# Performance work log

Measured on AMD Instinct MI355X. Metric: run time of the kernel, lower is better.

## Reference

```python
import jax, jax.numpy as jnp
import numpy as np

TOPK = 5
POWER = 1.01


def setup_inputs() -> dict:
    key = jax.random.key(0)
    k1, k2 = jax.random.split(key)
    B, C = 16384, 8192
    inp = jax.random.normal(k1, (B, C), dtype=jnp.float32)
    target = jax.random.randint(k2, (B,), 0, C, dtype=jnp.int64 if jax.config.jax_enable_x64 else jnp.int32)
    return {"input": inp, "target": target}


def reference(input, target):
    B = input.shape[0]
    rows = jnp.arange(B)
    # log(softmax(x)) == log_softmax(x)
    log_prob = jax.nn.log_softmax(input, axis=-1)  # [B, C]
    # top-k selection over classes
    topk_vals, topk_idx = jax.lax.top_k(input, TOPK)  # [B, K]
    # custom power-based softmax on the top-k subset
    exp_in = jnp.power(jnp.asarray(POWER, input.dtype), topk_vals)  # [B, K]
    log_prob_topk = jnp.log(exp_in / jnp.sum(exp_in, axis=-1, keepdims=True))
    # scatter the top-k log-probs back into a copy of log_prob
    log_prob_copy = log_prob.at[rows[:, None], topk_idx].set(log_prob_topk)
    # gather-based cross-entropy terms
    loss1 = jnp.mean(-log_prob[rows, target])
    loss2 = jnp.mean(-log_prob_copy[rows, target])
    return loss1 + loss2
```

## Files before the change

kernel.cpp:

```cpp
#include <hip/hip_runtime.h>

#define BLOCK 256
#define NCHUNK 8
#define NC 8192

__device__ __forceinline__ float fexp2(float x) { return __builtin_amdgcn_exp2f(x); }
__device__ __forceinline__ float flog2(float x) { return __builtin_amdgcn_logf(x); }

__device__ __forceinline__ void cas(float& hi, float& lo) {
    float h = fmaxf(hi, lo), l = fminf(hi, lo);
    hi = h; lo = l;
}

__device__ __forceinline__ void sort5(float& a0, float& a1, float& a2, float& a3, float& a4) {
    cas(a0, a1); cas(a3, a4); cas(a2, a4); cas(a2, a3); cas(a1, a4);
    cas(a0, a3); cas(a0, a2); cas(a1, a3); cas(a1, a2);
}

__device__ __forceinline__ void merge55(float& a0, float& a1, float& a2, float& a3, float& a4,
                                        float b0, float b1, float b2, float b3, float b4) {
    float L0 = fmaxf(a0, b4);
    float L1 = fmaxf(a1, b3);
    float L2 = fmaxf(a2, b2);
    float L3 = fmaxf(a3, b1);
    float L4 = fmaxf(a4, b0);
    sort5(L0, L1, L2, L3, L4);
    a0 = L0; a1 = L1; a2 = L2; a3 = L3; a4 = L4;
}

__global__ __launch_bounds__(BLOCK, 8) void ce_topk_rows(const float* __restrict__ inp,
                                                         const int* __restrict__ target,
                                                         float* __restrict__ row_loss) {
    constexpr float LOG2E  = 1.4426950408889634f;
    constexpr float LN2    = 0.6931471805599453f;
    constexpr float LN_P   = 0.009950330853155723f;
    constexpr float LOG2_P = 0.014355292977070041f;
    const float NI = -__builtin_inff();

    const int row  = blockIdx.x;
    const int tid  = threadIdx.x;
    const int lane = tid & 63;
    const int wav  = tid >> 6;
    const float* rp = inp + (size_t)row * NC;

    __shared__ float wsum[4];
    __shared__ float wtop[4][5];

    float xt = 0.f;
    if (tid == 0) xt = rp[target[row]];

    float4 c[NCHUNK];
    #pragma unroll
    for (int j = 0; j < NCHUNK; ++j)
        c[j] = reinterpret_cast<const float4*>(rp)[tid + BLOCK * j];

    float esA = 0.f, esB = 0.f;
    float a0, a1, a2, a3, a4;

    {
        float v0 = c[0].x, v1 = c[0].y, v2 = c[0].z, v3 = c[0].w;
        esA = fexp2(v0 * LOG2E) + fexp2(v1 * LOG2E);
        esB = fexp2(v2 * LOG2E) + fexp2(v3 * LOG2E);
        cas(v0, v1); cas(v2, v3); cas(v0, v2); cas(v1, v3); cas(v1, v2);
        a0 = v0; a1 = v1; a2 = v2; a3 = v3; a4 = NI;
    }

    #pragma unroll
    for (int j = 1; j < NCHUNK; ++j) {
        float v0 = c[j].x, v1 = c[j].y, v2 = c[j].z, v3 = c[j].w;
        esA += fexp2(v0 * LOG2E) + fexp2(v1 * LOG2E);
        esB += fexp2(v2 * LOG2E) + fexp2(v3 * LOG2E);
        cas(v0, v1); cas(v2, v3); cas(v0, v2); cas(v1, v3); cas(v1, v2);
        a1 = fmaxf(a1, v3);
        a2 = fmaxf(a2, v2);
        a3 = fmaxf(a3, v1);
        a4 = fmaxf(a4, v0);
        sort5(a0, a1, a2, a3, a4);
    }

    float es = esA + esB;
    #pragma unroll
    for (int o = 32; o > 0; o >>= 1) es += __shfl_xor(es, o, 64);

    #pragma unroll
    for (int o = 1; o < 64; o <<= 1) {
        float b0 = __shfl_xor(a0, o, 64);
        float b1 = __shfl_xor(a1, o, 64);
        float b2 = __shfl_xor(a2, o, 64);
        float b3 = __shfl_xor(a3, o, 64);
        float b4 = __shfl_xor(a4, o, 64);
        merge55(a0, a1, a2, a3, a4, b0, b1, b2, b3, b4);
    }

    if (lane == 0) {
        wsum[wav] = es;
        wtop[wav][0] = a0; wtop[wav][1] = a1; wtop[wav][2] = a2;
        wtop[wav][3] = a3; wtop[wav][4] = a4;
    }
    __syncthreads();

    if (tid == 0) {
        float s = wsum[0] + wsum[1] + wsum[2] + wsum[3];
        float A0 = wtop[0][0], A1 = wtop[0][1], A2 = wtop[0][2], A3 = wtop[0][3], A4 = wtop[0][4];
        #pragma unroll
        for (int w = 1; w < 4; ++w)
            merge55(A0, A1, A2, A3, A4,
                    wtop[w][0], wtop[w][1], wtop[w][2], wtop[w][3], wtop[w][4]);

        float spsum = fexp2(A0 * LOG2_P) + fexp2(A1 * LOG2_P) + fexp2(A2 * LOG2_P)
                    + fexp2(A3 * LOG2_P) + fexp2(A4 * LOG2_P);

        float lse  = LN2 * flog2(s);
        float l1   = lse - xt;
        float lsep = LN2 * flog2(spsum);
        bool found = (xt >= A4);
        float l2   = found ? (lsep - xt * LN_P) : l1;
        row_loss[row] = l1 + l2;
    }
}

__global__ __launch_bounds__(1024) void ce_topk_reduce(const float* __restrict__ rl,
                                                       float* __restrict__ out, int B) {
    float acc = 0.f;
    const float4* r4 = (const float4*)rl;
    const int n4 = B / 4;
    for (int i = threadIdx.x; i < n4; i += 1024) {
        float4 v = r4[i];
        acc += (v.x + v.y) + (v.z + v.w);
    }
    #pragma unroll
    for (int o = 32; o > 0; o >>= 1) acc += __shfl_xor(acc, o, 64);
    __shared__ float sr[16];
    if ((threadIdx.x & 63) == 0) sr[threadIdx.x >> 6] = acc;
    __syncthreads();
    if (threadIdx.x == 0) {
        float s = 0.f;
        #pragma unroll
        for (int w = 0; w < 16; ++w) s += sr[w];
        out[0] = s / (float)B;
    }
}

extern "C" void kernel_launch(void* const* d_in, const int* in_sizes, int n_in,
                              void* d_out, int out_size, void* d_ws, size_t ws_size,
                              hipStream_t stream) {
    const float* inp = (const float*)d_in[0];
    const int*   tgt = (const int*)d_in[1];
    const int B = in_sizes[1];
    float* rl = (float*)d_ws;
    ce_topk_rows<<<B, BLOCK, 0, stream>>>(inp, tgt, rl);
    ce_topk_reduce<<<1, 1024, 0, stream>>>(rl, (float*)d_out, B);
}
```

Before: 100.7 us.

## Process eight rows per block with register double-buffered prefetch of next row

```diff
diff --git a/kernel.cpp b/kernel.cpp
--- a/kernel.cpp
+++ b/kernel.cpp
@@ -1,8 +1,11 @@
 #include <hip/hip_runtime.h>
 
 #define BLOCK 256
-#define NCHUNK 8
 #define NC 8192
+#define ROWS 8
+#define NCH 8
+
+typedef float f4 __attribute__((ext_vector_type(4)));
 
 __device__ __forceinline__ float fexp2(float x) { return __builtin_amdgcn_exp2f(x); }
 __device__ __forceinline__ float flog2(float x) { return __builtin_amdgcn_logf(x); }
@@ -28,117 +31,130 @@
     a0 = L0; a1 = L1; a2 = L2; a3 = L3; a4 = L4;
 }
 
-__global__ __launch_bounds__(BLOCK, 8) void ce_topk_rows(const float* __restrict__ inp,
+__global__ __launch_bounds__(BLOCK, 6) void ce_topk_rows(const float* __restrict__ inp,
                                                          const int* __restrict__ target,
-                                                         float* __restrict__ row_loss) {
+                                                         float* __restrict__ part) {
     constexpr float LOG2E  = 1.4426950408889634f;
     constexpr float LN2    = 0.6931471805599453f;
     constexpr float LN_P   = 0.009950330853155723f;
     constexpr float LOG2_P = 0.014355292977070041f;
     const float NI = -__builtin_inff();
 
-    const int row  = blockIdx.x;
     const int tid  = threadIdx.x;
     const int lane = tid & 63;
     const int wav  = tid >> 6;
-    const float* rp = inp + (size_t)row * NC;
+    const int r0   = blockIdx.x * ROWS;
+    const float* base = inp + (size_t)r0 * NC;
 
-    __shared__ float wsum[4];
-    __shared__ float wtop[4][5];
+    __shared__ float wsum[2][4];
+    __shared__ float wtop[2][4][5];
 
     float xt = 0.f;
-    if (tid == 0) xt = rp[target[row]];
-
-    float4 c[NCHUNK];
-    #pragma unroll
-    for (int j = 0; j < NCHUNK; ++j)
-        c[j] = reinterpret_cast<const float4*>(rp)[tid + BLOCK * j];
-
-    float esA = 0.f, esB = 0.f;
-    float a0, a1, a2, a3, a4;
-
-    {
-        float v0 = c[0].x, v1 = c[0].y, v2 = c[0].z, v3 = c[0].w;
-        esA = fexp2(v0 * LOG2E) + fexp2(v1 * LOG2E);
-        esB = fexp2(v2 * LOG2E) + fexp2(v3 * LOG2E);
-        cas(v0, v1); cas(v2, v3); cas(v0, v2); cas(v1, v3); cas(v1, v2);
-        a0 = v0; a1 = v1; a2 = v2; a3 = v3; a4 = NI;
+    if (tid < ROWS) {
+        int t = target[r0 + tid];
+        xt = inp[(size_t)(r0 + tid) * NC + t];
     }
 
+    f4 buf[NCH];
     #pragma unroll
-    for (int j = 1; j < NCHUNK; ++j) {
-        float v0 = c[j].x, v1 = c[j].y, v2 = c[j].z, v3 = c[j].w;
-        esA += fexp2(v0 * LOG2E) + fexp2(v1 * LOG2E);
-        esB += fexp2(v2 * LOG2E) + fexp2(v3 * LOG2E);
-        cas(v0, v1); cas(v2, v3); cas(v0, v2); cas(v1, v3); cas(v1, v2);
-        a1 = fmaxf(a1, v3);
-        a2 = fmaxf(a2, v2);
-        a3 = fmaxf(a3, v1);
-        a4 = fmaxf(a4, v0);
-        sort5(a0, a1, a2, a3, a4);
+    for (int j = 0; j < NCH; ++j)
+        buf[j] = __builtin_nontemporal_load((const f4*)base + tid + BLOCK * j);
+
+    float myloss = 0.f;
+
+    for (int r = 0; r < ROWS; ++r) {
+        const f4* nxt = (const f4*)(base + (size_t)(r + 1) * NC) + tid;
+        const bool pre = (r + 1 < ROWS);
+
+        float es = 0.f;
+        float a0, a1, a2, a3, a4;
+
+        {
+            float v0 = buf[0][0], v1 = buf[0][1], v2 = buf[0][2], v3 = buf[0][3];
+            if (pre) buf[0] = __builtin_nontemporal_load(nxt);
+            es = (fexp2(v0 * LOG2E) + fexp2(v1 * LOG2E))
+               + (fexp2(v2 * LOG2E) + fexp2(v3 * LOG2E));
+            cas(v0, v1); cas(v2, v3); cas(v0, v2); cas(v1, v3); cas(v1, v2);
+            a0 = v0; a1 = v1; a2 = v2; a3 = v3; a4 = NI;
+        }
+
+        #pragma unroll
+        for (int j = 1; j < NCH; ++j) {
+            float v0 = buf[j][0], v1 = buf[j][1], v2 = buf[j][2], v3 = buf[j][3];
+            if (pre) buf[j] = __builtin_nontemporal_load(nxt + BLOCK * j);
+            es += (fexp2(v0 * LOG2E) + fexp2(v1 * LOG2E))
+                + (fexp2(v2 * LOG2E) + fexp2(v3 * LOG2E));
+            cas(v0, v1); cas(v2, v3); cas(v0, v2); cas(v1, v3); cas(v1, v2);
+            a1 = fmaxf(a1, v3);
+            a2 = fmaxf(a2, v2);
+            a3 = fmaxf(a3, v1);
+            a4 = fmaxf(a4, v0);
+            sort5(a0, a1, a2, a3, a4);
+        }
+
+        #pragma unroll
+        for (int o = 32; o > 0; o >>= 1) es += __shfl_xor(es, o, 64);
+
+        #pragma unroll
+        for (int o = 1; o < 64; o <<= 1) {
+            float b0 = __shfl_xor(a0, o, 64);
+            float b1 = __shfl_xor(a1, o, 64);
+            float b2 = __shfl_xor(a2, o, 64);
+            float b3 = __shfl_xor(a3, o, 64);
+            float b4 = __shfl_xor(a4, o, 64);
+            merge55(a0, a1, a2, a3, a4, b0, b1, b2, b3, b4);
+        }
+
+        const int p = r & 1;
+        if (lane == 0) {
+            wsum[p][wav] = es;
+            wtop[p][wav][0] = a0; wtop[p][wav][1] = a1; wtop[p][wav][2] = a2;
+            wtop[p][wav][3] = a3; wtop[p][wav][4] = a4;
+        }
+        __syncthreads();
+
+        if (tid == r) {
+            float s = wsum[p][0] + wsum[p][1] + wsum[p][2] + wsum[p][3];
+            float A0 = wtop[p][0][0], A1 = wtop[p][0][1], A2 = wtop[p][0][2],
+                  A3 = wtop[p][0][3], A4 = wtop[p][0][4];
+            #pragma unroll
+            for (int w = 1; w < 4; ++w)
+                merge55(A0, A1, A2, A3, A4,
+                        wtop[p][w][0], wtop[p][w][1], wtop[p][w][2],
+                        wtop[p][w][3], wtop[p][w][4]);
+
+            float spsum = fexp2(A0 * LOG2_P) + fexp2(A1 * LOG2_P) + fexp2(A2 * LOG2_P)
+                        + fexp2(A3 * LOG2_P) + fexp2(A4 * LOG2_P);
+
+            float lse  = LN2 * flog2(s);
+            float l1   = lse - xt;
+            float lsep = LN2 * flog2(spsum);
+            bool found = (xt >= A4);
+            float l2   = found ? (lsep - xt * LN_P) : l1;
+            myloss = l1 + l2;
+        }
     }
 
-    float es = esA + esB;
-    #pragma unroll
-    for (int o = 32; o > 0; o >>= 1) es += __shfl_xor(es, o, 64);
-
-    #pragma unroll
-    for (int o = 1; o < 64; o <<= 1) {
-        float b0 = __shfl_xor(a0, o, 64);
-        float b1 = __shfl_xor(a1, o, 64);
-        float b2 = __shfl_xor(a2, o, 64);
-        float b3 = __shfl_xor(a3, o, 64);
-        float b4 = __shfl_xor(a4, o, 64);
-        merge55(a0, a1, a2, a3, a4, b0, b1, b2, b3, b4);
-    }
-
-    if (lane == 0) {
-        wsum[wav] = es;
-        wtop[wav][0] = a0; wtop[wav][1] = a1; wtop[wav][2] = a2;
-        wtop[wav][3] = a3; wtop[wav][4] = a4;
-    }
-    __syncthreads();
-
-    if (tid == 0) {
-        float s = wsum[0] + wsum[1] + wsum[2] + wsum[3];
-        float A0 = wtop[0][0], A1 = wtop[0][1], A2 = wtop[0][2], A3 = wtop[0][3], A4 = wtop[0][4];
-        #pragma unroll
-        for (int w = 1; w < 4; ++w)
-            merge55(A0, A1, A2, A3, A4,
-                    wtop[w][0], wtop[w][1], wtop[w][2], wtop[w][3], wtop[w][4]);
-
-        float spsum = fexp2(A0 * LOG2_P) + fexp2(A1 * LOG2_P) + fexp2(A2 * LOG2_P)
-                    + fexp2(A3 * LOG2_P) + fexp2(A4 * LOG2_P);
-
-        float lse  = LN2 * flog2(s);
-        float l1   = lse - xt;
-        float lsep = LN2 * flog2(spsum);
-        bool found = (xt >= A4);
-        float l2   = found ? (lsep - xt * LN_P) : l1;
-        row_loss[row] = l1 + l2;
+    if (wav == 0) {
+        float l = myloss;
+        l += __shfl_xor(l, 1, 64);
+        l += __shfl_xor(l, 2, 64);
+        l += __shfl_xor(l, 4, 64);
+        if (lane == 0) part[blockIdx.x] = l;
     }
 }
 
-__global__ __launch_bounds__(1024) void ce_topk_reduce(const float* __restrict__ rl,
-                                                       float* __restrict__ out, int B) {
+__global__ __launch_bounds__(256) void ce_topk_reduce(const float* __restrict__ part,
+                                                      float* __restrict__ out, int nb, int B) {
     float acc = 0.f;
-    const float4* r4 = (const float4*)rl;
-    const int n4 = B / 4;
-    for (int i = threadIdx.x; i < n4; i += 1024) {
-        float4 v = r4[i];
-        acc += (v.x + v.y) + (v.z + v.w);
-    }
+    for (int i = threadIdx.x; i < nb; i += 256) acc += part[i];
     #pragma unroll
     for (int o = 32; o > 0; o >>= 1) acc += __shfl_xor(acc, o, 64);
-    __shared__ float sr[16];
+    __shared__ float sr[4];
     if ((threadIdx.x & 63) == 0) sr[threadIdx.x >> 6] = acc;
     __syncthreads();
-    if (threadIdx.x == 0) {
-        float s = 0.f;
-        #pragma unroll
-        for (int w = 0; w < 16; ++w) s += sr[w];
-        out[0] = s / (float)B;
-    }
+    if (threadIdx.x == 0)
+        out[0] = (sr[0] + sr[1] + sr[2] + sr[3]) / (float)B;
 }
 
 extern "C" void kernel_launch(void* const* d_in, const int* in_sizes, int n_in,
@@ -146,8 +162,9 @@
                               hipStream_t stream) {
     const float* inp = (const float*)d_in[0];
     const int*   tgt = (const int*)d_in[1];
-    const int B = in_sizes[1];
-    float* rl = (float*)d_ws;
-    ce_topk_rows<<<B, BLOCK, 0, stream>>>(inp, tgt, rl);
-    ce_topk_reduce<<<1, 1024, 0, stream>>>(rl, (float*)d_out, B);
+    const int B  = in_sizes[1];
+    const int nb = B / ROWS;
+    float* part = (float*)d_ws;
+    ce_topk_rows<<<nb, BLOCK, 0, stream>>>(inp, tgt, part);
+    ce_topk_reduce<<<1, 256, 0, stream>>>(part, (float*)d_out, nb, B);
 }
```

Measured after the change: 105.3 us. 4.6% more time.

## Fuse final reduction into row kernel via atomicAdd and drop reduce launch

Applied to the files above, without the earlier changes.

```diff
diff --git a/kernel.cpp b/kernel.cpp
--- a/kernel.cpp
+++ b/kernel.cpp
@@ -3,6 +3,9 @@
 #define BLOCK 256
 #define NCHUNK 8
 #define NC 8192
+#define INV_B 6.103515625e-05f
+
+typedef float f4 __attribute__((ext_vector_type(4)));
 
 __device__ __forceinline__ float fexp2(float x) { return __builtin_amdgcn_exp2f(x); }
 __device__ __forceinline__ float flog2(float x) { return __builtin_amdgcn_logf(x); }
@@ -28,9 +31,9 @@
     a0 = L0; a1 = L1; a2 = L2; a3 = L3; a4 = L4;
 }
 
-__global__ __launch_bounds__(BLOCK, 8) void ce_topk_rows(const float* __restrict__ inp,
+__global__ __launch_bounds__(BLOCK, 6) void ce_topk_rows(const float* __restrict__ inp,
                                                          const int* __restrict__ target,
-                                                         float* __restrict__ row_loss) {
+                                                         float* __restrict__ out) {
     constexpr float LOG2E  = 1.4426950408889634f;
     constexpr float LN2    = 0.6931471805599453f;
     constexpr float LN_P   = 0.009950330853155723f;
@@ -49,27 +52,27 @@
     float xt = 0.f;
     if (tid == 0) xt = rp[target[row]];
 
-    float4 c[NCHUNK];
+    f4 c[NCHUNK];
     #pragma unroll
     for (int j = 0; j < NCHUNK; ++j)
-        c[j] = reinterpret_cast<const float4*>(rp)[tid + BLOCK * j];
+        c[j] = reinterpret_cast<const f4*>(rp)[tid + BLOCK * j];
 
-    float esA = 0.f, esB = 0.f;
+    float es = 0.f;
     float a0, a1, a2, a3, a4;
 
     {
-        float v0 = c[0].x, v1 = c[0].y, v2 = c[0].z, v3 = c[0].w;
-        esA = fexp2(v0 * LOG2E) + fexp2(v1 * LOG2E);
-        esB = fexp2(v2 * LOG2E) + fexp2(v3 * LOG2E);
+        float v0 = c[0][0], v1 = c[0][1], v2 = c[0][2], v3 = c[0][3];
+        es = (fexp2(v0 * LOG2E) + fexp2(v1 * LOG2E))
+           + (fexp2(v2 * LOG2E) + fexp2(v3 * LOG2E));
         cas(v0, v1); cas(v2, v3); cas(v0, v2); cas(v1, v3); cas(v1, v2);
         a0 = v0; a1 = v1; a2 = v2; a3 = v3; a4 = NI;
     }
 
     #pragma unroll
     for (int j = 1; j < NCHUNK; ++j) {
-        float v0 = c[j].x, v1 = c[j].y, v2 = c[j].z, v3 = c[j].w;
-        esA += fexp2(v0 * LOG2E) + fexp2(v1 * LOG2E);
-        esB += fexp2(v2 * LOG2E) + fexp2(v3 * LOG2E);
+        float v0 = c[j][0], v1 = c[j][1], v2 = c[j][2], v3 = c[j][3];
+        es += (fexp2(v0 * LOG2E) + fexp2(v1 * LOG2E))
+            + (fexp2(v2 * LOG2E) + fexp2(v3 * LOG2E));
         cas(v0, v1); cas(v2, v3); cas(v0, v2); cas(v1, v3); cas(v1, v2);
         a1 = fmaxf(a1, v3);
         a2 = fmaxf(a2, v2);
@@ -78,7 +81,6 @@
         sort5(a0, a1, a2, a3, a4);
     }
 
-    float es = esA + esB;
     #pragma unroll
     for (int o = 32; o > 0; o >>= 1) es += __shfl_xor(es, o, 64);
 
@@ -115,29 +117,7 @@
         float lsep = LN2 * flog2(spsum);
         bool found = (xt >= A4);
         float l2   = found ? (lsep - xt * LN_P) : l1;
-        row_loss[row] = l1 + l2;
-    }
-}
-
-__global__ __launch_bounds__(1024) void ce_topk_reduce(const float* __restrict__ rl,
-                                                       float* __restrict__ out, int B) {
-    float acc = 0.f;
-    const float4* r4 = (const float4*)rl;
-    const int n4 = B / 4;
-    for (int i = threadIdx.x; i < n4; i += 1024) {
-        float4 v = r4[i];
-        acc += (v.x + v.y) + (v.z + v.w);
-    }
-    #pragma unroll
-    for (int o = 32; o > 0; o >>= 1) acc += __shfl_xor(acc, o, 64);
-    __shared__ float sr[16];
-    if ((threadIdx.x & 63) == 0) sr[threadIdx.x >> 6] = acc;
-    __syncthreads();
-    if (threadIdx.x == 0) {
-        float s = 0.f;
-        #pragma unroll
-        for (int w = 0; w < 16; ++w) s += sr[w];
-        out[0] = s / (float)B;
+        atomicAdd(out, (l1 + l2) * INV_B);
     }
 }
 
@@ -147,7 +127,7 @@
     const float* inp = (const float*)d_in[0];
     const int*   tgt = (const int*)d_in[1];
     const int B = in_sizes[1];
-    float* rl = (float*)d_ws;
-    ce_topk_rows<<<B, BLOCK, 0, stream>>>(inp, tgt, rl);
-    ce_topk_reduce<<<1, 1024, 0, stream>>>(rl, (float*)d_out, B);
+    float* out = (float*)d_out;
+    hipMemsetAsync(out, 0, sizeof(float), stream);
+    ce_topk_rows<<<B, BLOCK, 0, stream>>>(inp, tgt, out);
 }
```

Result: slower. 238.5 us (+136.8%).
